# Kernel optimization log

Hardware: AMD Instinct MI355X
Metric: run time of the kernel (lower is better)

The kernel has to match this reference:

```python
import jax, jax.numpy as jnp
import numpy as np

N = 50000        # node_num
E = 1600000      # num edges
F_IN = 8
HID = 1000
R = 100          # robustness_length


def setup_inputs() -> dict:
    key = jax.random.key(0)
    ks = jax.random.split(key, 16)
    X = jax.random.normal(ks[0], (N, F_IN), dtype=jnp.float32)
    edge_index = jax.random.randint(ks[1], (2, E), 0, N, dtype=jnp.int64)
    s = 1.0 / np.sqrt(F_IN)
    # SAGEConv mean-aggr params (PyG: out = lin_l(aggr) + lin_r(x), lin_r has no bias)
    lin_l_w = jax.random.uniform(ks[2], (1, F_IN), jnp.float32, -s, s)
    lin_l_b = jax.random.uniform(ks[3], (1,), jnp.float32, -s, s)
    lin_r_w = jax.random.uniform(ks[4], (1, F_IN), jnp.float32, -s, s)
    # SAGEConv max-aggr params
    lin_l1_w = jax.random.uniform(ks[5], (1, F_IN), jnp.float32, -s, s)
    lin_l1_b = jax.random.uniform(ks[6], (1,), jnp.float32, -s, s)
    lin_r1_w = jax.random.uniform(ks[7], (1, F_IN), jnp.float32, -s, s)
    # MLP params
    s0 = 1.0 / np.sqrt(N)
    W0 = jax.random.uniform(ks[8], (HID, N), jnp.float32, -s0, s0)
    b0 = jax.random.uniform(ks[9], (HID,), jnp.float32, -s0, s0)
    s1 = 1.0 / np.sqrt(HID)
    W1 = jax.random.uniform(ks[10], (HID, HID), jnp.float32, -s1, s1)
    b1 = jax.random.uniform(ks[11], (HID,), jnp.float32, -s1, s1)
    W2 = jax.random.uniform(ks[12], (R, HID), jnp.float32, -s1, s1)
    b2 = jax.random.uniform(ks[13], (R,), jnp.float32, -s1, s1)
    return dict(X=X, edge_index=edge_index,
                lin_l_w=lin_l_w, lin_l_b=lin_l_b, lin_r_w=lin_r_w,
                lin_l1_w=lin_l1_w, lin_l1_b=lin_l1_b, lin_r1_w=lin_r1_w,
                W0=W0, b0=b0, W1=W1, b1=b1, W2=W2, b2=b2)


def reference(X, edge_index, lin_l_w, lin_l_b, lin_r_w,
              lin_l1_w, lin_l1_b, lin_r1_w,
              W0, b0, W1, b1, W2, b2):
    src, dst = edge_index[0], edge_index[1]
    msgs = X[src]  # [E, F_IN] gathered neighbor features
    cnt = jax.ops.segment_sum(jnp.ones((E,), jnp.float32), dst, num_segments=N)
    # mean aggregation (empty -> 0)
    agg_mean = jax.ops.segment_sum(msgs, dst, num_segments=N) / jnp.maximum(cnt, 1.0)[:, None]
    # max aggregation (empty -> 0, per PyG scatter-max fill)
    agg_max = jax.ops.segment_max(msgs, dst, num_segments=N)
    agg_max = jnp.where(cnt[:, None] > 0, agg_max, 0.0)
    # SAGEConv: lin_l(aggr) + lin_r(x)
    h_mean = jax.nn.relu(agg_mean @ lin_l_w.T + lin_l_b + X @ lin_r_w.T)   # [N,1]
    h_max = jax.nn.relu(agg_max @ lin_l1_w.T + lin_l1_b + X @ lin_r1_w.T)  # [N,1]
    x = (h_mean + h_max).reshape(-1)  # [N]
    X_embedding = x
    h = jax.nn.relu(W0 @ x + b0)
    h = jax.nn.relu(W1 @ h + b1)
    out = jax.nn.relu(W2 @ h + b2)
    return (X_embedding, out)
```

## Files before the change

kernel.cpp:

```cpp
#include <hip/hip_runtime.h>

#define N_NODES 50000
#define N_EDGES 1600000
#define F_IN 8
#define HID 1000
#define R_OUT 100

#define BSHIFT 6
#define NPB 64
#define NB 782
#define CAP_B 2400
#define CHUNK 4096
#define NBIN_BLOCKS ((N_EDGES + CHUNK - 1) / CHUNK)
#define NCHUNK0 25


__device__ __forceinline__ unsigned fkey(float f) {
    unsigned b = __float_as_uint(f);
    return (b & 0x80000000u) ? ~b : (b | 0x80000000u);
}
__device__ __forceinline__ float funkey(unsigned k) {
    unsigned b = (k & 0x80000000u) ? (k & 0x7fffffffu) : ~k;
    return __uint_as_float(b);
}

__global__ void init_ws(unsigned* __restrict__ p, int n) {
    int i = blockIdx.x * blockDim.x + threadIdx.x;
    if (i < n) p[i] = 0u;
}

__global__ void bin_kernel(const int* __restrict__ ei,
                           const float* __restrict__ X,
                           const float* __restrict__ wl,
                           int* __restrict__ cursor,
                           unsigned* __restrict__ binned,
                           int* __restrict__ ovf_cnt,
                           float* __restrict__ ovf_sum,
                           unsigned* __restrict__ ovf_max) {
    __shared__ unsigned sEntry[CHUNK];
    __shared__ unsigned short sBucket[CHUNK];
    __shared__ int hist[NB];
    __shared__ int pos[NB];
    __shared__ int base[NB];
    int tid = threadIdx.x;
    int e0 = blockIdx.x * CHUNK;
    int e1 = e0 + CHUNK;
    if (e1 > N_EDGES) e1 = N_EDGES;
    int ne = e1 - e0;

    for (int i = tid; i < NB; i += 256) { hist[i] = 0; pos[i] = 0; }
    __syncthreads();

    for (int j = tid; j < ne; j += 256) {
        int src = ei[e0 + j];
        int dst = ei[N_EDGES + e0 + j];
        int b = dst >> BSHIFT;
        sEntry[j] = (unsigned)src | ((unsigned)(dst & (NPB - 1)) << 16);
        sBucket[j] = (unsigned short)b;
        atomicAdd(&hist[b], 1);
    }
    __syncthreads();

    for (int b = tid; b < NB; b += 256) {
        int h = hist[b];
        base[b] = (h > 0) ? atomicAdd(&cursor[b], h) : 0;
    }
    __syncthreads();

    for (int j = tid; j < ne; j += 256) {
        unsigned entry = sEntry[j];
        int b = sBucket[j];
        int p = atomicAdd(&pos[b], 1);
        int gp = base[b] + p;
        if (gp < CAP_B) {
            binned[(size_t)b * CAP_B + gp] = entry;
        } else {
            int src = entry & 0xFFFF;
            int dst = b * NPB + (int)(entry >> 16);
            const float4* X4 = (const float4*)(X + src * F_IN);
            float4 a = X4[0], bb = X4[1];
            float f[8] = {a.x, a.y, a.z, a.w, bb.x, bb.y, bb.z, bb.w};
            float d = 0.f;
#pragma unroll
            for (int k = 0; k < 8; ++k) d += f[k] * wl[k];
            atomicAdd(&ovf_cnt[dst], 1);
            atomicAdd(&ovf_sum[dst], d);
            unsigned* mb = ovf_max + (size_t)dst * 8;
#pragma unroll
            for (int k = 0; k < 8; ++k) atomicMax(&mb[k], fkey(f[k]));
        }
    }
}

__global__ void agg_kernel(const int* __restrict__ cursor,
                           const unsigned* __restrict__ binned,
                           const int* __restrict__ ovf_cnt,
                           const float* __restrict__ ovf_sum,
                           const unsigned* __restrict__ ovf_max,
                           const float* __restrict__ X,
                           const float* __restrict__ lin_l_w,
                           const float* __restrict__ lin_l_b,
                           const float* __restrict__ lin_r_w,
                           const float* __restrict__ lin_l1_w,
                           const float* __restrict__ lin_l1_b,
                           const float* __restrict__ lin_r1_w,
                           float* __restrict__ xemb) {
    __shared__ unsigned sEntry[CAP_B];
    __shared__ unsigned sSorted[CAP_B];
    __shared__ int sCnt[NPB];
    __shared__ int sOff[NPB];
    __shared__ int sPos[NPB];

    int b = blockIdx.x;
    int tid = threadIdx.x;
    int n = cursor[b];
    if (n > CAP_B) n = CAP_B;

    if (tid < NPB) { sCnt[tid] = 0; sPos[tid] = 0; }
    __syncthreads();

    for (int j = tid; j < n; j += 256) {
        unsigned e = binned[(size_t)b * CAP_B + j];
        sEntry[j] = e;
        atomicAdd(&sCnt[e >> 16], 1);
    }
    __syncthreads();

    if (tid == 0) {
        int run = 0;
#pragma unroll
        for (int i = 0; i < NPB; ++i) { sOff[i] = run; run += sCnt[i]; }
    }
    __syncthreads();

    for (int j = tid; j < n; j += 256) {
        unsigned e = sEntry[j];
        int d = e >> 16;
        int p = atomicAdd(&sPos[d], 1);
        sSorted[sOff[d] + p] = e;
    }
    __syncthreads();

    int nl = tid >> 2;
    int r = tid & 3;
    int beg = sOff[nl];
    int cnt = sCnt[nl];

    float wl[8];
#pragma unroll
    for (int k = 0; k < 8; ++k) wl[k] = lin_l_w[k];

    float sumdot = 0.f;
    float mx[8];
#pragma unroll
    for (int k = 0; k < 8; ++k) mx[k] = -INFINITY;

    for (int j = beg + r; j < beg + cnt; j += 4) {
        int src = sSorted[j] & 0xFFFF;
        const float4* X4 = (const float4*)(X + src * F_IN);
        float4 a = X4[0], bb = X4[1];
        float f[8] = {a.x, a.y, a.z, a.w, bb.x, bb.y, bb.z, bb.w};
        float d = 0.f;
#pragma unroll
        for (int k = 0; k < 8; ++k) d += f[k] * wl[k];
        sumdot += d;
#pragma unroll
        for (int k = 0; k < 8; ++k) mx[k] = fmaxf(mx[k], f[k]);
    }
#pragma unroll
    for (int m = 1; m <= 2; m <<= 1) {
        sumdot += __shfl_xor(sumdot, m, 4);
#pragma unroll
        for (int k = 0; k < 8; ++k) mx[k] = fmaxf(mx[k], __shfl_xor(mx[k], m, 4));
    }

    if (r == 0) {
        int node = b * NPB + nl;
        if (node < N_NODES) {
            int oc = ovf_cnt[node];
            int total = cnt + oc;
            float sd = sumdot + ovf_sum[node];
            if (oc > 0) {
                const unsigned* mb = ovf_max + (size_t)node * 8;
#pragma unroll
                for (int k = 0; k < 8; ++k) mx[k] = fmaxf(mx[k], funkey(mb[k]));
            }
            float c = (float)total;
            float mean_dot = sd / fmaxf(c, 1.0f);
            const float4* X4 = (const float4*)(X + node * F_IN);
            float4 a = X4[0], bb = X4[1];
            float f[8] = {a.x, a.y, a.z, a.w, bb.x, bb.y, bb.z, bb.w};
            float dr = 0.f, dr1 = 0.f, dmax = 0.f;
            bool nonempty = (total > 0);
#pragma unroll
            for (int k = 0; k < 8; ++k) {
                float m = nonempty ? mx[k] : 0.0f;
                dmax += m * lin_l1_w[k];
                dr   += f[k] * lin_r_w[k];
                dr1  += f[k] * lin_r1_w[k];
            }
            float hm = fmaxf(mean_dot + lin_l_b[0] + dr, 0.f);
            float hx = fmaxf(dmax + lin_l1_b[0] + dr1, 0.f);
            xemb[node] = hm + hx;
        }
    }
}


template <int BLOCK, int NCHUNK>
__global__ void gemv_partial(const float* __restrict__ W,
                             const float* __restrict__ x,
                             float* __restrict__ part, int cols) {
    int row = blockIdx.x;
    int c = blockIdx.y;
    int chunk = cols / NCHUNK;
    const float4* W4 = (const float4*)(W + (size_t)row * cols + (size_t)c * chunk);
    const float4* x4 = (const float4*)(x + c * chunk);
    int n4 = chunk >> 2;
    float s = 0.f;
    for (int j = threadIdx.x; j < n4; j += BLOCK) {
        float4 w = W4[j], xx = x4[j];
        s += w.x * xx.x + w.y * xx.y + w.z * xx.z + w.w * xx.w;
    }
#pragma unroll
    for (int off = 32; off > 0; off >>= 1) s += __shfl_down(s, off, 64);
    __shared__ float red[BLOCK / 64];
    int t = threadIdx.x;
    if ((t & 63) == 0) red[t >> 6] = s;
    __syncthreads();
    if (t == 0) {
        float tot = 0.f;
#pragma unroll
        for (int w = 0; w < BLOCK / 64; ++w) tot += red[w];
        part[row * NCHUNK + c] = tot;
    }
}

template <int NCHUNK>
__global__ void gemv_finalize(const float* __restrict__ part,
                              const float* __restrict__ bias,
                              float* __restrict__ y, int rows) {
    int r = blockIdx.x * blockDim.x + threadIdx.x;
    if (r >= rows) return;
    float s = 0.f;
#pragma unroll
    for (int c = 0; c < NCHUNK; ++c) s += part[r * NCHUNK + c];
    y[r] = fmaxf(s + bias[r], 0.f);
}

template <int BLOCK>
__global__ void gemv_relu(const float* __restrict__ W,
                          const float* __restrict__ x,
                          const float* __restrict__ bias,
                          float* __restrict__ y, int cols) {
    int row = blockIdx.x;
    const float4* W4 = (const float4*)(W + (size_t)row * cols);
    const float4* x4 = (const float4*)x;
    int n4 = cols >> 2;
    float s = 0.f;
    for (int j = threadIdx.x; j < n4; j += BLOCK) {
        float4 w = W4[j], xx = x4[j];
        s += w.x * xx.x + w.y * xx.y + w.z * xx.z + w.w * xx.w;
    }
#pragma unroll
    for (int off = 32; off > 0; off >>= 1) s += __shfl_down(s, off, 64);
    __shared__ float red[BLOCK / 64];
    int t = threadIdx.x;
    if ((t & 63) == 0) red[t >> 6] = s;
    __syncthreads();
    if (t == 0) {
        float tot = 0.f;
#pragma unroll
        for (int w = 0; w < BLOCK / 64; ++w) tot += red[w];
        y[row] = fmaxf(tot + bias[row], 0.f);
    }
}


__global__ void edge_kernel_fb(const int* __restrict__ ei,
                               const float* __restrict__ X,
                               const float* __restrict__ wl,
                               float* __restrict__ sumw,
                               float* __restrict__ cnt,
                               unsigned* __restrict__ maxb) {
    int e = blockIdx.x * blockDim.x + threadIdx.x;
    if (e >= N_EDGES) return;
    int src = ei[e];
    int dst = ei[N_EDGES + e];
    const float4* X4 = (const float4*)(X + src * F_IN);
    float4 a = X4[0], b = X4[1];
    float f[8] = {a.x, a.y, a.z, a.w, b.x, b.y, b.z, b.w};
    float d = 0.f;
#pragma unroll
    for (int k = 0; k < 8; ++k) d += f[k] * wl[k];
    atomicAdd(&sumw[dst], d);
    atomicAdd(&cnt[dst], 1.0f);
    unsigned* mb = maxb + (size_t)dst * 8;
#pragma unroll
    for (int k = 0; k < 8; ++k) atomicMax(&mb[k], fkey(f[k]));
}

__global__ void node_kernel_fb(const float* __restrict__ X,
                               const float* __restrict__ sumw,
                               const float* __restrict__ cnt,
                               const unsigned* __restrict__ maxb,
                               const float* __restrict__ lin_l_b,
                               const float* __restrict__ lin_r_w,
                               const float* __restrict__ lin_l1_w,
                               const float* __restrict__ lin_l1_b,
                               const float* __restrict__ lin_r1_w,
                               float* __restrict__ xout) {
    int i = blockIdx.x * blockDim.x + threadIdx.x;
    if (i >= N_NODES) return;
    float c = cnt[i];
    float mean_dot = sumw[i] / fmaxf(c, 1.0f);
    const float4* X4 = (const float4*)(X + i * F_IN);
    float4 a = X4[0], b = X4[1];
    float f[8] = {a.x, a.y, a.z, a.w, b.x, b.y, b.z, b.w};
    const uint4* M4 = (const uint4*)(maxb + (size_t)i * 8);
    uint4 m0 = M4[0], m1 = M4[1];
    unsigned mk[8] = {m0.x, m0.y, m0.z, m0.w, m1.x, m1.y, m1.z, m1.w};
    float dr = 0.f, dr1 = 0.f, dmax = 0.f;
    bool nonempty = (c > 0.f);
#pragma unroll
    for (int k = 0; k < 8; ++k) {
        float mxv = nonempty ? funkey(mk[k]) : 0.0f;
        dmax += mxv * lin_l1_w[k];
        dr   += f[k] * lin_r_w[k];
        dr1  += f[k] * lin_r1_w[k];
    }
    float hm = fmaxf(mean_dot + lin_l_b[0] + dr, 0.f);
    float hx = fmaxf(dmax + lin_l1_b[0] + dr1, 0.f);
    xout[i] = hm + hx;
}


extern "C" void kernel_launch(void* const* d_in, const int* in_sizes, int n_in,
                              void* d_out, int out_size, void* d_ws, size_t ws_size,
                              hipStream_t stream) {
    const float* X        = (const float*)d_in[0];
    const int*   ei       = (const int*)d_in[1];
    const float* lin_l_w  = (const float*)d_in[2];
    const float* lin_l_b  = (const float*)d_in[3];
    const float* lin_r_w  = (const float*)d_in[4];
    const float* lin_l1_w = (const float*)d_in[5];
    const float* lin_l1_b = (const float*)d_in[6];
    const float* lin_r1_w = (const float*)d_in[7];
    const float* W0       = (const float*)d_in[8];
    const float* b0       = (const float*)d_in[9];
    const float* W1       = (const float*)d_in[10];
    const float* b1       = (const float*)d_in[11];
    const float* W2       = (const float*)d_in[12];
    const float* b2       = (const float*)d_in[13];

    float* xemb = (float*)d_out;
    float* out2 = xemb + N_NODES;

    const size_t zero_words = (size_t)NB + (size_t)N_NODES * 10;
    const size_t need_words = zero_words + (size_t)NB * CAP_B
                              + (size_t)HID * NCHUNK0 + 2 * HID;
    if (ws_size >= need_words * 4) {
        int*      cursor  = (int*)d_ws;
        int*      ovf_cnt = cursor + NB;
        float*    ovf_sum = (float*)(ovf_cnt + N_NODES);
        unsigned* ovf_max = (unsigned*)(ovf_sum + N_NODES);
        unsigned* binned  = ovf_max + (size_t)N_NODES * 8;
        float*    part0   = (float*)(binned + (size_t)NB * CAP_B);
        float*    h0      = part0 + HID * NCHUNK0;
        float*    h1      = h0 + HID;

        hipLaunchKernelGGL(init_ws, dim3(((int)zero_words + 255) / 256), dim3(256), 0, stream,
                           (unsigned*)d_ws, (int)zero_words);
        hipLaunchKernelGGL(bin_kernel, dim3(NBIN_BLOCKS), dim3(256), 0, stream,
                           ei, X, lin_l_w, cursor, binned, ovf_cnt, ovf_sum, ovf_max);
        hipLaunchKernelGGL(agg_kernel, dim3(NB), dim3(256), 0, stream,
                           cursor, binned, ovf_cnt, ovf_sum, ovf_max, X,
                           lin_l_w, lin_l_b, lin_r_w, lin_l1_w, lin_l1_b, lin_r1_w, xemb);

        hipLaunchKernelGGL((gemv_partial<256, NCHUNK0>), dim3(HID, NCHUNK0), dim3(256), 0, stream,
                           W0, xemb, part0, N_NODES);
        hipLaunchKernelGGL(gemv_finalize<NCHUNK0>, dim3((HID + 255) / 256), dim3(256), 0, stream,
                           part0, b0, h0, HID);
        hipLaunchKernelGGL(gemv_relu<256>, dim3(HID), dim3(256), 0, stream,
                           W1, h0, b1, h1, HID);
        hipLaunchKernelGGL(gemv_relu<256>, dim3(R_OUT), dim3(256), 0, stream,
                           W2, h1, b2, out2, HID);
    } else {
        float*    sumw = (float*)d_ws;
        float*    cntf = sumw + N_NODES;
        unsigned* maxb = (unsigned*)(cntf + N_NODES);
        float*    h0   = (float*)(maxb + (size_t)N_NODES * 8);
        float*    h1   = h0 + HID;

        int zw = N_NODES * 10;
        hipLaunchKernelGGL(init_ws, dim3((zw + 255) / 256), dim3(256), 0, stream,
                           (unsigned*)d_ws, zw);
        hipLaunchKernelGGL(edge_kernel_fb, dim3((N_EDGES + 255) / 256), dim3(256), 0, stream,
                           ei, X, lin_l_w, sumw, cntf, maxb);
        hipLaunchKernelGGL(node_kernel_fb, dim3((N_NODES + 255) / 256), dim3(256), 0, stream,
                           X, sumw, cntf, maxb, lin_l_b, lin_r_w, lin_l1_w, lin_l1_b,
                           lin_r1_w, xemb);
        hipLaunchKernelGGL(gemv_relu<256>, dim3(HID), dim3(256), 0, stream,
                           W0, xemb, b0, h0, N_NODES);
        hipLaunchKernelGGL(gemv_relu<256>, dim3(HID), dim3(256), 0, stream,
                           W1, h0, b1, h1, HID);
        hipLaunchKernelGGL(gemv_relu<256>, dim3(R_OUT), dim3(256), 0, stream,
                           W2, h1, b2, out2, HID);
    }
}
```

Measured before the change: 359.6 us.

## Double agg bin size and fold GEMV0 finalize into atomic accumulation

Doubles nodes per aggregation bin (128 nodes, 391 bins, 512-thread agg blocks) so fewer, larger blocks handle the per-bin sort and reduce. The first-layer GEMV now atomically adds chunk partials into h0, pre-seeded with bias b0 in the init kernel. The ReLU moves into the next GEMV's input load, which removes the finalize kernel and the partial buffer. Atomic float accumulation makes the result order-dependent, and larger bins raise shared-memory use per block.

Result: no change. 358.1 us (-0.4%).

```diff
diff --git a/kernel.cpp b/kernel.cpp
--- a/kernel.cpp
+++ b/kernel.cpp
@@ -6,10 +6,10 @@
 #define HID 1000
 #define R_OUT 100
 
-#define BSHIFT 6
-#define NPB 64
-#define NB 782
-#define CAP_B 2400
+#define BSHIFT 7
+#define NPB 128
+#define NB 391
+#define CAP_B 4608
 #define CHUNK 4096
 #define NBIN_BLOCKS ((N_EDGES + CHUNK - 1) / CHUNK)
 #define NCHUNK0 25
@@ -24,9 +24,11 @@
     return __uint_as_float(b);
 }
 
-__global__ void init_ws(unsigned* __restrict__ p, int n) {
+__global__ void init_kernel(unsigned* __restrict__ p, int nzero,
+                            const float* __restrict__ b0, float* __restrict__ h0) {
     int i = blockIdx.x * blockDim.x + threadIdx.x;
-    if (i < n) p[i] = 0u;
+    if (i < nzero) p[i] = 0u;
+    if (i < HID) h0[i] = b0[i];
 }
 
 __global__ void bin_kernel(const int* __restrict__ ei,
@@ -119,7 +121,7 @@
     if (tid < NPB) { sCnt[tid] = 0; sPos[tid] = 0; }
     __syncthreads();
 
-    for (int j = tid; j < n; j += 256) {
+    for (int j = tid; j < n; j += 512) {
         unsigned e = binned[(size_t)b * CAP_B + j];
         sEntry[j] = e;
         atomicAdd(&sCnt[e >> 16], 1);
@@ -133,7 +135,7 @@
     }
     __syncthreads();
 
-    for (int j = tid; j < n; j += 256) {
+    for (int j = tid; j < n; j += 512) {
         unsigned e = sEntry[j];
         int d = e >> 16;
         int p = atomicAdd(&sPos[d], 1);
@@ -208,11 +210,11 @@
 
 
 template <int BLOCK, int NCHUNK>
-__global__ void gemv_partial(const float* __restrict__ W,
-                             const float* __restrict__ x,
-                             float* __restrict__ part, int cols) {
-    int row = blockIdx.x;
-    int c = blockIdx.y;
+__global__ void gemv_accum(const float* __restrict__ W,
+                           const float* __restrict__ x,
+                           float* __restrict__ y, int cols) {
+    int c = blockIdx.x;
+    int row = blockIdx.y;
     int chunk = cols / NCHUNK;
     const float4* W4 = (const float4*)(W + (size_t)row * cols + (size_t)c * chunk);
     const float4* x4 = (const float4*)(x + c * chunk);
@@ -232,23 +234,11 @@
         float tot = 0.f;
 #pragma unroll
         for (int w = 0; w < BLOCK / 64; ++w) tot += red[w];
-        part[row * NCHUNK + c] = tot;
-    }
-}
-
-template <int NCHUNK>
-__global__ void gemv_finalize(const float* __restrict__ part,
-                              const float* __restrict__ bias,
-                              float* __restrict__ y, int rows) {
-    int r = blockIdx.x * blockDim.x + threadIdx.x;
-    if (r >= rows) return;
-    float s = 0.f;
-#pragma unroll
-    for (int c = 0; c < NCHUNK; ++c) s += part[r * NCHUNK + c];
-    y[r] = fmaxf(s + bias[r], 0.f);
-}
-
-template <int BLOCK>
+        atomicAdd(&y[row], tot);
+    }
+}
+
+template <int BLOCK, bool RELUX>
 __global__ void gemv_relu(const float* __restrict__ W,
                           const float* __restrict__ x,
                           const float* __restrict__ bias,
@@ -260,6 +250,10 @@
     float s = 0.f;
     for (int j = threadIdx.x; j < n4; j += BLOCK) {
         float4 w = W4[j], xx = x4[j];
+        if (RELUX) {
+            xx.x = fmaxf(xx.x, 0.f); xx.y = fmaxf(xx.y, 0.f);
+            xx.z = fmaxf(xx.z, 0.f); xx.w = fmaxf(xx.w, 0.f);
+        }
         s += w.x * xx.x + w.y * xx.y + w.z * xx.z + w.w * xx.w;
     }
 #pragma unroll
@@ -276,6 +270,11 @@
     }
 }
 
+
+__global__ void init_ws_fb(unsigned* __restrict__ p, int n) {
+    int i = blockIdx.x * blockDim.x + threadIdx.x;
+    if (i < n) p[i] = 0u;
+}
 
 __global__ void edge_kernel_fb(const int* __restrict__ ei,
                                const float* __restrict__ X,
@@ -357,33 +356,29 @@
     float* out2 = xemb + N_NODES;
 
     const size_t zero_words = (size_t)NB + (size_t)N_NODES * 10;
-    const size_t need_words = zero_words + (size_t)NB * CAP_B
-                              + (size_t)HID * NCHUNK0 + 2 * HID;
+    const size_t need_words = zero_words + (size_t)NB * CAP_B + 2 * HID;
     if (ws_size >= need_words * 4) {
         int*      cursor  = (int*)d_ws;
         int*      ovf_cnt = cursor + NB;
         float*    ovf_sum = (float*)(ovf_cnt + N_NODES);
         unsigned* ovf_max = (unsigned*)(ovf_sum + N_NODES);
         unsigned* binned  = ovf_max + (size_t)N_NODES * 8;
-        float*    part0   = (float*)(binned + (size_t)NB * CAP_B);
-        float*    h0      = part0 + HID * NCHUNK0;
+        float*    h0      = (float*)(binned + (size_t)NB * CAP_B);
         float*    h1      = h0 + HID;
 
-        hipLaunchKernelGGL(init_ws, dim3(((int)zero_words + 255) / 256), dim3(256), 0, stream,
-                           (unsigned*)d_ws, (int)zero_words);
+        hipLaunchKernelGGL(init_kernel, dim3(((int)zero_words + 255) / 256), dim3(256), 0, stream,
+                           (unsigned*)d_ws, (int)zero_words, b0, h0);
         hipLaunchKernelGGL(bin_kernel, dim3(NBIN_BLOCKS), dim3(256), 0, stream,
                            ei, X, lin_l_w, cursor, binned, ovf_cnt, ovf_sum, ovf_max);
-        hipLaunchKernelGGL(agg_kernel, dim3(NB), dim3(256), 0, stream,
+        hipLaunchKernelGGL(agg_kernel, dim3(NB), dim3(512), 0, stream,
                            cursor, binned, ovf_cnt, ovf_sum, ovf_max, X,
                            lin_l_w, lin_l_b, lin_r_w, lin_l1_w, lin_l1_b, lin_r1_w, xemb);
 
-        hipLaunchKernelGGL((gemv_partial<256, NCHUNK0>), dim3(HID, NCHUNK0), dim3(256), 0, stream,
-                           W0, xemb, part0, N_NODES);
-        hipLaunchKernelGGL(gemv_finalize<NCHUNK0>, dim3((HID + 255) / 256), dim3(256), 0, stream,
-                           part0, b0, h0, HID);
-        hipLaunchKernelGGL(gemv_relu<256>, dim3(HID), dim3(256), 0, stream,
+        hipLaunchKernelGGL((gemv_accum<256, NCHUNK0>), dim3(NCHUNK0, HID), dim3(256), 0, stream,
+                           W0, xemb, h0, N_NODES);
+        hipLaunchKernelGGL((gemv_relu<256, true>), dim3(HID), dim3(256), 0, stream,
                            W1, h0, b1, h1, HID);
-        hipLaunchKernelGGL(gemv_relu<256>, dim3(R_OUT), dim3(256), 0, stream,
+        hipLaunchKernelGGL((gemv_relu<256, false>), dim3(R_OUT), dim3(256), 0, stream,
                            W2, h1, b2, out2, HID);
     } else {
         float*    sumw = (float*)d_ws;
@@ -393,18 +388,18 @@
         float*    h1   = h0 + HID;
 
         int zw = N_NODES * 10;
-        hipLaunchKernelGGL(init_ws, dim3((zw + 255) / 256), dim3(256), 0, stream,
+        hipLaunchKernelGGL(init_ws_fb, dim3((zw + 255) / 256), dim3(256), 0, stream,
                            (unsigned*)d_ws, zw);
         hipLaunchKernelGGL(edge_kernel_fb, dim3((N_EDGES + 255) / 256), dim3(256), 0, stream,
                            ei, X, lin_l_w, sumw, cntf, maxb);
         hipLaunchKernelGGL(node_kernel_fb, dim3((N_NODES + 255) / 256), dim3(256), 0, stream,
                            X, sumw, cntf, maxb, lin_l_b, lin_r_w, lin_l1_w, lin_l1_b,
                            lin_r1_w, xemb);
-        hipLaunchKernelGGL(gemv_relu<256>, dim3(HID), dim3(256), 0, stream,
+        hipLaunchKernelGGL((gemv_relu<256, false>), dim3(HID), dim3(256), 0, stream,
                            W0, xemb, b0, h0, N_NODES);
-        hipLaunchKernelGGL(gemv_relu<256>, dim3(HID), dim3(256), 0, stream,
+        hipLaunchKernelGGL((gemv_relu<256, false>), dim3(HID), dim3(256), 0, stream,
                            W1, h0, b1, h1, HID);
-        hipLaunchKernelGGL(gemv_relu<256>, dim3(R_OUT), dim3(256), 0, stream,
+        hipLaunchKernelGGL((gemv_relu<256, false>), dim3(R_OUT), dim3(256), 0, stream,
                            W2, h1, b2, out2, HID);
     }
 }
```
